# Kernel tuning notes

Hardware: AMD Instinct MI355X
Metric: run time of the kernel (lower is better)

## Reference

```python
import jax, jax.numpy as jnp
import numpy as np

N_NODES = 100000
N_EDGES = 20000
NNZ = 800000
D_IN = 256
D_OUT = 256


def _segment_mean(feats, seg_ids, num_segments):
    # feats: [nnz, d] gathered features; seg_ids: [nnz] target segment per entry
    s = jax.ops.segment_sum(feats, seg_ids, num_segments=num_segments)
    cnt = jax.ops.segment_sum(jnp.ones((seg_ids.shape[0],), feats.dtype), seg_ids,
                              num_segments=num_segments)
    return s / jnp.maximum(cnt, 1.0)[:, None]


def setup_inputs() -> dict:
    key = jax.random.key(0)
    k1, k2, k3, k4, k5 = jax.random.split(key, 5)
    X = jax.random.normal(k1, (N_NODES, D_IN), dtype=jnp.float32)
    W = jax.random.normal(k2, (D_IN, D_OUT), dtype=jnp.float32) * (1.0 / np.sqrt(D_IN))
    b = jax.random.normal(k3, (D_OUT,), dtype=jnp.float32) * 0.01
    vertex_idx = jax.random.randint(k4, (NNZ,), 0, N_NODES, dtype=jnp.int32)
    edge_idx = jax.random.randint(k5, (NNZ,), 0, N_EDGES, dtype=jnp.int32)
    return {"X": X, "W": W, "b": b, "vertex_idx": vertex_idx, "edge_idx": edge_idx}


def reference(X, W, b, vertex_idx, edge_idx):
    # theta: linear projection
    H = X @ W + b                                   # [N_NODES, D_OUT]
    # v2e mean: hyperedge feature = mean of incident vertex features
    Y = _segment_mean(H[vertex_idx], edge_idx, N_EDGES)   # [N_EDGES, D_OUT]
    # e2v mean: vertex feature = mean of incident hyperedge features
    X_ = _segment_mean(Y[edge_idx], vertex_idx, N_NODES)  # [N_NODES, D_OUT]
    # ReLU; dropout is identity in eval mode
    return jax.nn.relu(X_)
```

## Files before the change

kernel.cpp:

```cpp
#include <hip/hip_runtime.h>
#include <hip/hip_bf16.h>

constexpr int N_NODES = 100000;
constexpr int N_EDGES = 20000;
constexpr int NNZ     = 800000;
constexpr int D       = 256;

typedef unsigned short ushort_t;
typedef unsigned short ushort4v __attribute__((ext_vector_type(4)));
typedef unsigned short ushort8v __attribute__((ext_vector_type(8)));
typedef __bf16         bf16x8   __attribute__((ext_vector_type(8)));
typedef float          f32x4    __attribute__((ext_vector_type(4)));
typedef float          f32x8    __attribute__((ext_vector_type(8)));

static __device__ inline ushort_t f2bf(float f) {
  unsigned u = __builtin_bit_cast(unsigned, f);
  return (ushort_t)((u + 0x7FFFu + ((u >> 16) & 1u)) >> 16);
}

static __device__ inline f32x8 row_f32(const ushort_t* p) {
  bf16x8 b = __builtin_bit_cast(bf16x8, *(const ushort8v*)p);
  return __builtin_convertvector(b, f32x8);
}

static __device__ inline int bsum(unsigned long long x) {
  return (int)((x * 0x0101010101010101ULL) >> 56);
}

constexpr int HCHUNKS   = 8;
constexpr int CHUNK     = NNZ / HCHUNKS;
constexpr int CHUNK4    = CHUNK / 4;
constexpr int NH_RANGES = 5;
constexpr int NH_BINS   = N_NODES / NH_RANGES;
constexpr int NH_BLOCKS = NH_RANGES * HCHUNKS;
constexpr int EH_BLOCKS = HCHUNKS;
constexpr int HIST_BLOCKS  = NH_BLOCKS + EH_BLOCKS;
constexpr int TRANS_BLOCKS = 64;
constexpr int CAST_BLOCKS  = 6250;
constexpr int PREP_BLOCKS  = HIST_BLOCKS + TRANS_BLOCKS + CAST_BLOCKS;
constexpr int HWORDS = 5000;

__global__ __launch_bounds__(256) void prep_kernel(
    const float* __restrict__ X, const float* __restrict__ W,
    const int* __restrict__ vidx, const int* __restrict__ eidx,
    ushort_t* __restrict__ Xb, ushort_t* __restrict__ Wt,
    unsigned char* __restrict__ pe, unsigned char* __restrict__ pn,
    unsigned char* __restrict__ lre, unsigned char* __restrict__ lrn) {
  __shared__ unsigned int hist[HWORDS];
  const int blk = blockIdx.x, tid = threadIdx.x;
  if (blk < HIST_BLOCKS) {
    const bool is_n = blk < NH_BLOCKS;
    const int c  = is_n ? (blk & 7) : (blk - NH_BLOCKS);
    const int lo = is_n ? (blk >> 3) * NH_BINS : 0;
    const int* __restrict__ idx = is_n ? vidx : eidx;
    unsigned char* __restrict__ lr = is_n ? lrn : lre;
    for (int t = tid; t < HWORDS; t += 256) hist[t] = 0;
    __syncthreads();
    const int base4 = c * CHUNK4;
#pragma unroll 2
    for (int k = tid; k < CHUNK4; k += 256) {
      int i4 = base4 + k;
      int4 q = ((const int4*)idx)[i4];
      int vv[4] = {q.x, q.y, q.z, q.w};
#pragma unroll
      for (int j = 0; j < 4; ++j) {
        unsigned rel = (unsigned)(vv[j] - lo);
        if (rel < (unsigned)NH_BINS) {
          unsigned sh = 8u * (rel & 3u);
          unsigned old = atomicAdd(&hist[rel >> 2], 1u << sh);
          lr[(size_t)i4 * 4 + j] = (unsigned char)((old >> sh) & 0xFFu);
        }
      }
    }
    __syncthreads();
    unsigned char* __restrict__ pb = is_n ? pn : pe;
    for (int t = tid; t < NH_BINS; t += 256) {
      unsigned byte = (hist[t >> 2] >> (8u * (t & 3u))) & 0xFFu;
      pb[(size_t)(lo + t) * 8 + c] = (unsigned char)byte;
    }
  } else if (blk < HIST_BLOCKS + TRANS_BLOCKS) {
    int wb = blk - HIST_BLOCKS;
#pragma unroll
    for (int i = 0; i < 4; ++i) {
      int k = wb * 4 + i;
      Wt[(size_t)tid * 256 + k] = f2bf(W[(size_t)k * 256 + tid]);
    }
  } else {
    int cb = blk - HIST_BLOCKS - TRANS_BLOCKS;
#pragma unroll
    for (int q = 0; q < 4; ++q) {
      int idx4 = cb * 1024 + q * 256 + tid;
      float4 v = ((const float4*)X)[idx4];
      ushort4v o = { f2bf(v.x), f2bf(v.y), f2bf(v.z), f2bf(v.w) };
      *(ushort4v*)&Xb[(size_t)idx4 * 4] = o;
    }
  }
}

constexpr int SCAN_L    = N_EDGES + N_NODES;
constexpr int SCAN_TPB  = 1024;
constexpr int SCAN_EPT  = 4;
constexpr int SCAN_TILE = SCAN_TPB * SCAN_EPT;
constexpr int SCAN_NB   = (SCAN_L + SCAN_TILE - 1) / SCAN_TILE;

__global__ __launch_bounds__(1024) void scan_phaseA(
    const unsigned long long* __restrict__ pe,
    const unsigned long long* __restrict__ pn,
    int* __restrict__ comb, int* __restrict__ btot) {
  __shared__ int wsum[16];
  const int tid = threadIdx.x, lane = tid & 63, wid = tid >> 6;
  const int base = blockIdx.x * SCAN_TILE + tid * SCAN_EPT;
  int v[SCAN_EPT];
#pragma unroll
  for (int i = 0; i < SCAN_EPT; ++i) {
    int j = base + i;
    int x = 0;
    if (j < SCAN_L) x = bsum(j < N_EDGES ? pe[j] : pn[j - N_EDGES]);
    v[i] = x;
  }
  int tsum = v[0] + v[1] + v[2] + v[3];
  int x = tsum;
#pragma unroll
  for (int d = 1; d < 64; d <<= 1) {
    int y = __shfl_up(x, (unsigned)d, 64);
    if (lane >= d) x += y;
  }
  if (lane == 63) wsum[wid] = x;
  __syncthreads();
  if (wid == 0) {
    int s = (lane < 16) ? wsum[lane] : 0;
#pragma unroll
    for (int d = 1; d < 16; d <<= 1) {
      int y = __shfl_up(s, (unsigned)d, 64);
      if (lane >= d) s += y;
    }
    if (lane < 16) wsum[lane] = s;
  }
  __syncthreads();
  int texcl = ((wid == 0) ? 0 : wsum[wid - 1]) + (x - tsum);
  int run = texcl;
#pragma unroll
  for (int i = 0; i < SCAN_EPT; ++i) {
    int j = base + i;
    if (j < SCAN_L) comb[j] = run;
    run += v[i];
  }
  if (tid == 0) btot[blockIdx.x] = wsum[15];
}

__global__ __launch_bounds__(1024) void scan_phaseC(
    const int* __restrict__ comb, const int* __restrict__ btot,
    int* __restrict__ eoff, int* __restrict__ noff) {
  int add = 0;
  for (int bdx = 0; bdx < blockIdx.x; ++bdx) add += btot[bdx];
  const int base = blockIdx.x * SCAN_TILE + threadIdx.x * SCAN_EPT;
#pragma unroll
  for (int i = 0; i < SCAN_EPT; ++i) {
    int j = base + i;
    if (j < SCAN_L) {
      int val = comb[j] + add;
      if (j < N_EDGES) eoff[j] = val;
      else             noff[j - N_EDGES] = val - NNZ;
    }
  }
  if (blockIdx.x == 0 && threadIdx.x == 0) {
    eoff[N_EDGES] = NNZ;
    noff[N_NODES] = NNZ;
  }
}

__global__ __launch_bounds__(256) void scatter_calc(
    const int* __restrict__ vidx, const int* __restrict__ eidx,
    const int* __restrict__ eoff, const int* __restrict__ noff,
    const unsigned long long* __restrict__ pe,
    const unsigned long long* __restrict__ pn,
    const unsigned char* __restrict__ lre, const unsigned char* __restrict__ lrn,
    int* __restrict__ evals, int* __restrict__ nvals) {
  int i4 = blockIdx.x * 256 + threadIdx.x;
  if (i4 >= NNZ / 4) return;
  int c = i4 / CHUNK4;
  unsigned long long mask = (1ULL << (8 * c)) - 1ULL;
  int4 e4 = ((const int4*)eidx)[i4];
  int4 v4 = ((const int4*)vidx)[i4];
  unsigned le = *(const unsigned*)(lre + (size_t)i4 * 4);
  unsigned ln = *(const unsigned*)(lrn + (size_t)i4 * 4);
  int ee[4] = {e4.x, e4.y, e4.z, e4.w};
  int vv[4] = {v4.x, v4.y, v4.z, v4.w};
#pragma unroll
  for (int j = 0; j < 4; ++j) {
    int e = ee[j], v = vv[j];
    int re = (int)((le >> (8 * j)) & 0xFFu);
    int rn = (int)((ln >> (8 * j)) & 0xFFu);
    evals[eoff[e] + bsum(pe[e] & mask) + re] = v;
    nvals[noff[v] + bsum(pn[v] & mask) + rn] = e;
  }
}

__global__ __launch_bounds__(256) void v2e_mean(
    const ushort_t* __restrict__ Xb, const int* __restrict__ eoff,
    const int* __restrict__ evals, ushort_t* __restrict__ Xeb, int nseg) {
  int lane = threadIdx.x & 63;
  int half = lane >> 5, l32 = lane & 31;
  int seg  = blockIdx.x * 4 + (threadIdx.x >> 6);
  if (seg >= nseg) return;
  int s = eoff[seg], e = eoff[seg + 1];
  f32x8 acc = {0, 0, 0, 0, 0, 0, 0, 0};
  int j = s + half;
  for (; j + 6 < e; j += 8) {
    int r0 = evals[j], r1 = evals[j + 2], r2 = evals[j + 4], r3 = evals[j + 6];
    f32x8 f0 = row_f32(&Xb[(size_t)r0 * 256 + l32 * 8]);
    f32x8 f1 = row_f32(&Xb[(size_t)r1 * 256 + l32 * 8]);
    f32x8 f2 = row_f32(&Xb[(size_t)r2 * 256 + l32 * 8]);
    f32x8 f3 = row_f32(&Xb[(size_t)r3 * 256 + l32 * 8]);
    acc += (f0 + f1) + (f2 + f3);
  }
  for (; j < e; j += 2)
    acc += row_f32(&Xb[(size_t)evals[j] * 256 + l32 * 8]);
  float r[8];
#pragma unroll
  for (int i = 0; i < 8; ++i) r[i] = acc[i] + __shfl_down(acc[i], 32);
  if (half == 0) {
    float inv = 1.0f / (float)max(e - s, 1);
    ushort8v o;
#pragma unroll
    for (int i = 0; i < 8; ++i) o[i] = f2bf(r[i] * inv);
    *(ushort8v*)&Xeb[(size_t)seg * 256 + l32 * 8] = o;
  }
}

__global__ __launch_bounds__(256) void gemm_mfma(
    const ushort_t* __restrict__ A, const ushort_t* __restrict__ Wt,
    const float* __restrict__ bias, ushort_t* __restrict__ Ye) {
  const int w = threadIdx.x >> 6, lane = threadIdx.x & 63;
  const int m15 = lane & 15, q = lane >> 4;
  const int m0 = blockIdx.x * 16;
  const ushort_t* arow = A + (size_t)(m0 + m15) * 256 + q * 8;
  f32x4 acc[4] = { {0,0,0,0}, {0,0,0,0}, {0,0,0,0}, {0,0,0,0} };
  for (int k0 = 0; k0 < 256; k0 += 32) {
    bf16x8 af = __builtin_bit_cast(bf16x8, *(const ushort8v*)(arow + k0));
#pragma unroll
    for (int t = 0; t < 4; ++t) {
      const ushort_t* brow = Wt + (size_t)(w * 64 + t * 16 + m15) * 256 + k0 + q * 8;
      bf16x8 bf = __builtin_bit_cast(bf16x8, *(const ushort8v*)brow);
      acc[t] = __builtin_amdgcn_mfma_f32_16x16x32_bf16(af, bf, acc[t], 0, 0, 0);
    }
  }
#pragma unroll
  for (int t = 0; t < 4; ++t) {
    int col = w * 64 + t * 16 + m15;
    float bv = bias[col];
#pragma unroll
    for (int r = 0; r < 4; ++r) {
      int row = m0 + q * 4 + r;
      Ye[(size_t)row * 256 + col] = f2bf(acc[t][r] + bv);
    }
  }
}

__global__ __launch_bounds__(256) void e2v_mean_relu(
    const ushort_t* __restrict__ Yeb, const int* __restrict__ noff,
    const int* __restrict__ nvals, float* __restrict__ dst, int nseg) {
  int lane = threadIdx.x & 63;
  int half = lane >> 5, l32 = lane & 31;
  int seg  = blockIdx.x * 4 + (threadIdx.x >> 6);
  if (seg >= nseg) return;
  int s = noff[seg], e = noff[seg + 1];
  f32x8 acc = {0, 0, 0, 0, 0, 0, 0, 0};
  int j = s + half;
  for (; j + 6 < e; j += 8) {
    int r0 = nvals[j], r1 = nvals[j + 2], r2 = nvals[j + 4], r3 = nvals[j + 6];
    f32x8 f0 = row_f32(&Yeb[(size_t)r0 * 256 + l32 * 8]);
    f32x8 f1 = row_f32(&Yeb[(size_t)r1 * 256 + l32 * 8]);
    f32x8 f2 = row_f32(&Yeb[(size_t)r2 * 256 + l32 * 8]);
    f32x8 f3 = row_f32(&Yeb[(size_t)r3 * 256 + l32 * 8]);
    acc += (f0 + f1) + (f2 + f3);
  }
  for (; j < e; j += 2)
    acc += row_f32(&Yeb[(size_t)nvals[j] * 256 + l32 * 8]);
  float r[8];
#pragma unroll
  for (int i = 0; i < 8; ++i) r[i] = acc[i] + __shfl_down(acc[i], 32);
  if (half == 0) {
    float inv = 1.0f / (float)max(e - s, 1);
    float4 o0, o1;
    o0.x = fmaxf(r[0] * inv, 0.f); o0.y = fmaxf(r[1] * inv, 0.f);
    o0.z = fmaxf(r[2] * inv, 0.f); o0.w = fmaxf(r[3] * inv, 0.f);
    o1.x = fmaxf(r[4] * inv, 0.f); o1.y = fmaxf(r[5] * inv, 0.f);
    o1.z = fmaxf(r[6] * inv, 0.f); o1.w = fmaxf(r[7] * inv, 0.f);
    size_t base = (size_t)seg * 256 + l32 * 8;
    *(float4*)&dst[base]     = o0;
    *(float4*)&dst[base + 4] = o1;
  }
}

constexpr size_t OFF_XB    = 0;
constexpr size_t OFF_XEB   = OFF_XB  + (size_t)N_NODES * D * 2;
constexpr size_t OFF_YEB   = OFF_XEB + (size_t)N_EDGES * D * 2;
constexpr size_t OFF_WT    = OFF_YEB + (size_t)N_EDGES * D * 2;
constexpr size_t OFF_PE    = OFF_WT  + (size_t)D * D * 2;
constexpr size_t OFF_PN    = OFF_PE  + (size_t)N_EDGES * 8;
constexpr size_t OFF_LRE   = OFF_PN  + (size_t)N_NODES * 8;
constexpr size_t OFF_LRN   = OFF_LRE + (size_t)NNZ;
constexpr size_t OFF_EOFF  = OFF_LRN + (size_t)NNZ;
constexpr size_t OFF_NOFF  = OFF_EOFF + (size_t)(N_EDGES + 1 + 3) * 4;
constexpr size_t OFF_EVALS = OFF_NOFF + (size_t)(N_NODES + 1 + 3) * 4;
constexpr size_t OFF_NVALS = OFF_EVALS + (size_t)NNZ * 4;
constexpr size_t OFF_COMB  = OFF_NVALS + (size_t)NNZ * 4;
constexpr size_t OFF_BTOT  = OFF_COMB + (size_t)SCAN_L * 4;

extern "C" void kernel_launch(void* const* d_in, const int* in_sizes, int n_in,
                              void* d_out, int out_size, void* d_ws, size_t ws_size,
                              hipStream_t stream) {
  const float* X    = (const float*)d_in[0];
  const float* W    = (const float*)d_in[1];
  const float* b    = (const float*)d_in[2];
  const int*   vidx = (const int*)d_in[3];
  const int*   eidx = (const int*)d_in[4];
  float*       out  = (float*)d_out;

  char* ws = (char*)d_ws;
  ushort_t* Xb   = (ushort_t*)(ws + OFF_XB);
  ushort_t* Xeb  = (ushort_t*)(ws + OFF_XEB);
  ushort_t* Yeb  = (ushort_t*)(ws + OFF_YEB);
  ushort_t* Wt   = (ushort_t*)(ws + OFF_WT);
  unsigned char* pe_b = (unsigned char*)(ws + OFF_PE);
  unsigned char* pn_b = (unsigned char*)(ws + OFF_PN);
  unsigned long long* pe_u = (unsigned long long*)(ws + OFF_PE);
  unsigned long long* pn_u = (unsigned long long*)(ws + OFF_PN);
  unsigned char* lre = (unsigned char*)(ws + OFF_LRE);
  unsigned char* lrn = (unsigned char*)(ws + OFF_LRN);
  int* eoff  = (int*)(ws + OFF_EOFF);
  int* noff  = (int*)(ws + OFF_NOFF);
  int* evals = (int*)(ws + OFF_EVALS);
  int* nvals = (int*)(ws + OFF_NVALS);
  int* comb  = (int*)(ws + OFF_COMB);
  int* btot  = (int*)(ws + OFF_BTOT);


  prep_kernel<<<PREP_BLOCKS, 256, 0, stream>>>(X, W, vidx, eidx, Xb, Wt,
                                               pe_b, pn_b, lre, lrn);

  scan_phaseA<<<SCAN_NB, SCAN_TPB, 0, stream>>>(pe_u, pn_u, comb, btot);
  scan_phaseC<<<SCAN_NB, SCAN_TPB, 0, stream>>>(comb, btot, eoff, noff);

  scatter_calc<<<(NNZ / 4 + 255) / 256, 256, 0, stream>>>(
      vidx, eidx, eoff, noff, pe_u, pn_u, lre, lrn, evals, nvals);

  v2e_mean<<<(N_EDGES + 3) / 4, 256, 0, stream>>>(Xb, eoff, evals, Xeb, N_EDGES);

  gemm_mfma<<<N_EDGES / 16, 256, 0, stream>>>(Xeb, Wt, b, Yeb);

  e2v_mean_relu<<<(N_NODES + 3) / 4, 256, 0, stream>>>(Yeb, noff, nvals, out, N_NODES);
}
```

Measured before the change: 423.9 us.

## Widen histogram chunking to 32 and split segment-mean kernels into column quarters

Histogram construction now uses 32 chunks instead of 8, giving more blocks for the counting-sort prep. The per-(segment, chunk) prefix bytes grow to four u64 words, so the scan and scatter read and mask four words. Both segment-mean kernels are restructured: each wave handles a 64-column quarter of a segment, with 8 lanes per row and 8 rows in flight, and a 4x larger grid. This is meant to expose more parallelism and more memory-level parallelism on the gathers. The cost is more index re-reads, a larger prefix table, and extra shuffle reductions.

```diff
diff --git a/kernel.cpp b/kernel.cpp
--- a/kernel.cpp
+++ b/kernel.cpp
@@ -12,6 +12,8 @@
 typedef __bf16         bf16x8   __attribute__((ext_vector_type(8)));
 typedef float          f32x4    __attribute__((ext_vector_type(4)));
 typedef float          f32x8    __attribute__((ext_vector_type(8)));
+typedef unsigned long long u64;
+typedef unsigned long long u64x2 __attribute__((ext_vector_type(2)));
 
 static __device__ inline ushort_t f2bf(float f) {
   unsigned u = __builtin_bit_cast(unsigned, f);
@@ -23,13 +25,13 @@
   return __builtin_convertvector(b, f32x8);
 }
 
-static __device__ inline int bsum(unsigned long long x) {
+static __device__ inline int bsum(u64 x) {
   return (int)((x * 0x0101010101010101ULL) >> 56);
 }
 
-constexpr int HCHUNKS   = 8;
-constexpr int CHUNK     = NNZ / HCHUNKS;
-constexpr int CHUNK4    = CHUNK / 4;
+constexpr int HCHUNKS   = 32;
+constexpr int CHUNK4    = NNZ / 4 / HCHUNKS;
+constexpr int PWORDS    = HCHUNKS / 8;
 constexpr int NH_RANGES = 5;
 constexpr int NH_BINS   = N_NODES / NH_RANGES;
 constexpr int NH_BLOCKS = NH_RANGES * HCHUNKS;
@@ -50,14 +52,13 @@
   const int blk = blockIdx.x, tid = threadIdx.x;
   if (blk < HIST_BLOCKS) {
     const bool is_n = blk < NH_BLOCKS;
-    const int c  = is_n ? (blk & 7) : (blk - NH_BLOCKS);
-    const int lo = is_n ? (blk >> 3) * NH_BINS : 0;
+    const int c  = is_n ? (blk & (HCHUNKS - 1)) : (blk - NH_BLOCKS);
+    const int lo = is_n ? (blk >> 5) * NH_BINS : 0;
     const int* __restrict__ idx = is_n ? vidx : eidx;
     unsigned char* __restrict__ lr = is_n ? lrn : lre;
     for (int t = tid; t < HWORDS; t += 256) hist[t] = 0;
     __syncthreads();
     const int base4 = c * CHUNK4;
-#pragma unroll 2
     for (int k = tid; k < CHUNK4; k += 256) {
       int i4 = base4 + k;
       int4 q = ((const int4*)idx)[i4];
@@ -76,7 +77,7 @@
     unsigned char* __restrict__ pb = is_n ? pn : pe;
     for (int t = tid; t < NH_BINS; t += 256) {
       unsigned byte = (hist[t >> 2] >> (8u * (t & 3u))) & 0xFFu;
-      pb[(size_t)(lo + t) * 8 + c] = (unsigned char)byte;
+      pb[(size_t)(lo + t) * HCHUNKS + c] = (unsigned char)byte;
     }
   } else if (blk < HIST_BLOCKS + TRANS_BLOCKS) {
     int wb = blk - HIST_BLOCKS;
@@ -103,9 +104,14 @@
 constexpr int SCAN_TILE = SCAN_TPB * SCAN_EPT;
 constexpr int SCAN_NB   = (SCAN_L + SCAN_TILE - 1) / SCAN_TILE;
 
+static __device__ inline int bsum32(const u64* P) {
+  u64x2 a = *(const u64x2*)P;
+  u64x2 b = *(const u64x2*)(P + 2);
+  return bsum(a[0]) + bsum(a[1]) + bsum(b[0]) + bsum(b[1]);
+}
+
 __global__ __launch_bounds__(1024) void scan_phaseA(
-    const unsigned long long* __restrict__ pe,
-    const unsigned long long* __restrict__ pn,
+    const u64* __restrict__ pe, const u64* __restrict__ pn,
     int* __restrict__ comb, int* __restrict__ btot) {
   __shared__ int wsum[16];
   const int tid = threadIdx.x, lane = tid & 63, wid = tid >> 6;
@@ -115,7 +121,9 @@
   for (int i = 0; i < SCAN_EPT; ++i) {
     int j = base + i;
     int x = 0;
-    if (j < SCAN_L) x = bsum(j < N_EDGES ? pe[j] : pn[j - N_EDGES]);
+    if (j < SCAN_L)
+      x = bsum32(j < N_EDGES ? pe + (size_t)j * PWORDS
+                             : pn + (size_t)(j - N_EDGES) * PWORDS);
     v[i] = x;
   }
   int tsum = v[0] + v[1] + v[2] + v[3];
@@ -172,14 +180,18 @@
 __global__ __launch_bounds__(256) void scatter_calc(
     const int* __restrict__ vidx, const int* __restrict__ eidx,
     const int* __restrict__ eoff, const int* __restrict__ noff,
-    const unsigned long long* __restrict__ pe,
-    const unsigned long long* __restrict__ pn,
+    const u64* __restrict__ pe, const u64* __restrict__ pn,
     const unsigned char* __restrict__ lre, const unsigned char* __restrict__ lrn,
     int* __restrict__ evals, int* __restrict__ nvals) {
   int i4 = blockIdx.x * 256 + threadIdx.x;
   if (i4 >= NNZ / 4) return;
   int c = i4 / CHUNK4;
-  unsigned long long mask = (1ULL << (8 * c)) - 1ULL;
+  int w = c >> 3, sub = c & 7;
+  u64 mw = (1ULL << (8 * sub)) - 1ULL;
+  u64 m0 = (w > 0) ? ~0ULL : mw;
+  u64 m1 = (w > 1) ? ~0ULL : ((w == 1) ? mw : 0ULL);
+  u64 m2 = (w > 2) ? ~0ULL : ((w == 2) ? mw : 0ULL);
+  u64 m3 = (w == 3) ? mw : 0ULL;
   int4 e4 = ((const int4*)eidx)[i4];
   int4 v4 = ((const int4*)vidx)[i4];
   unsigned le = *(const unsigned*)(lre + (size_t)i4 * 4);
@@ -189,42 +201,46 @@
 #pragma unroll
   for (int j = 0; j < 4; ++j) {
     int e = ee[j], v = vv[j];
+    u64x2 ea = *(const u64x2*)(pe + (size_t)e * PWORDS);
+    u64x2 eb = *(const u64x2*)(pe + (size_t)e * PWORDS + 2);
+    u64x2 na = *(const u64x2*)(pn + (size_t)v * PWORDS);
+    u64x2 nb = *(const u64x2*)(pn + (size_t)v * PWORDS + 2);
+    int pre_e = bsum(ea[0] & m0) + bsum(ea[1] & m1) + bsum(eb[0] & m2) + bsum(eb[1] & m3);
+    int pre_n = bsum(na[0] & m0) + bsum(na[1] & m1) + bsum(nb[0] & m2) + bsum(nb[1] & m3);
     int re = (int)((le >> (8 * j)) & 0xFFu);
     int rn = (int)((ln >> (8 * j)) & 0xFFu);
-    evals[eoff[e] + bsum(pe[e] & mask) + re] = v;
-    nvals[noff[v] + bsum(pn[v] & mask) + rn] = e;
-  }
-}
-
-__global__ __launch_bounds__(256) void v2e_mean(
+    evals[eoff[e] + pre_e + re] = v;
+    nvals[noff[v] + pre_n + rn] = e;
+  }
+}
+
+constexpr int V2E_NBLK = N_EDGES / 4;
+__global__ __launch_bounds__(256) void v2e_mean_q(
     const ushort_t* __restrict__ Xb, const int* __restrict__ eoff,
-    const int* __restrict__ evals, ushort_t* __restrict__ Xeb, int nseg) {
-  int lane = threadIdx.x & 63;
-  int half = lane >> 5, l32 = lane & 31;
-  int seg  = blockIdx.x * 4 + (threadIdx.x >> 6);
-  if (seg >= nseg) return;
+    const int* __restrict__ evals, ushort_t* __restrict__ Xeb) {
+  int q    = blockIdx.x / V2E_NBLK;
+  int blk  = blockIdx.x - q * V2E_NBLK;
+  int wave = threadIdx.x >> 6, lane = threadIdx.x & 63;
+  int g = lane >> 3, l8 = lane & 7;
+  int seg = blk * 4 + wave;
   int s = eoff[seg], e = eoff[seg + 1];
+  const ushort_t* base = Xb + q * 64 + l8 * 8;
   f32x8 acc = {0, 0, 0, 0, 0, 0, 0, 0};
-  int j = s + half;
-  for (; j + 6 < e; j += 8) {
-    int r0 = evals[j], r1 = evals[j + 2], r2 = evals[j + 4], r3 = evals[j + 6];
-    f32x8 f0 = row_f32(&Xb[(size_t)r0 * 256 + l32 * 8]);
-    f32x8 f1 = row_f32(&Xb[(size_t)r1 * 256 + l32 * 8]);
-    f32x8 f2 = row_f32(&Xb[(size_t)r2 * 256 + l32 * 8]);
-    f32x8 f3 = row_f32(&Xb[(size_t)r3 * 256 + l32 * 8]);
-    acc += (f0 + f1) + (f2 + f3);
-  }
-  for (; j < e; j += 2)
-    acc += row_f32(&Xb[(size_t)evals[j] * 256 + l32 * 8]);
-  float r[8];
-#pragma unroll
-  for (int i = 0; i < 8; ++i) r[i] = acc[i] + __shfl_down(acc[i], 32);
-  if (half == 0) {
+#pragma unroll 2
+  for (int j = s + g; j < e; j += 8)
+    acc += row_f32(&base[(size_t)evals[j] * 256]);
+#pragma unroll
+  for (int i = 0; i < 8; ++i) {
+    acc[i] += __shfl_xor(acc[i], 8, 64);
+    acc[i] += __shfl_xor(acc[i], 16, 64);
+    acc[i] += __shfl_xor(acc[i], 32, 64);
+  }
+  if (g == 0) {
     float inv = 1.0f / (float)max(e - s, 1);
     ushort8v o;
 #pragma unroll
-    for (int i = 0; i < 8; ++i) o[i] = f2bf(r[i] * inv);
-    *(ushort8v*)&Xeb[(size_t)seg * 256 + l32 * 8] = o;
+    for (int i = 0; i < 8; ++i) o[i] = f2bf(acc[i] * inv);
+    *(ushort8v*)&Xeb[(size_t)seg * 256 + q * 64 + l8 * 8] = o;
   }
 }
 
@@ -257,39 +273,37 @@
   }
 }
 
-__global__ __launch_bounds__(256) void e2v_mean_relu(
+constexpr int E2V_NBLK = N_NODES / 4;
+__global__ __launch_bounds__(256) void e2v_mean_relu_q(
     const ushort_t* __restrict__ Yeb, const int* __restrict__ noff,
-    const int* __restrict__ nvals, float* __restrict__ dst, int nseg) {
-  int lane = threadIdx.x & 63;
-  int half = lane >> 5, l32 = lane & 31;
-  int seg  = blockIdx.x * 4 + (threadIdx.x >> 6);
-  if (seg >= nseg) return;
+    const int* __restrict__ nvals, float* __restrict__ dst) {
+  int q    = blockIdx.x / E2V_NBLK;
+  int blk  = blockIdx.x - q * E2V_NBLK;
+  int wave = threadIdx.x >> 6, lane = threadIdx.x & 63;
+  int g = lane >> 3, l8 = lane & 7;
+  int seg = blk * 4 + wave;
   int s = noff[seg], e = noff[seg + 1];
+  const ushort_t* base = Yeb + q * 64 + l8 * 8;
   f32x8 acc = {0, 0, 0, 0, 0, 0, 0, 0};
-  int j = s + half;
-  for (; j + 6 < e; j += 8) {
-    int r0 = nvals[j], r1 = nvals[j + 2], r2 = nvals[j + 4], r3 = nvals[j + 6];
-    f32x8 f0 = row_f32(&Yeb[(size_t)r0 * 256 + l32 * 8]);
-    f32x8 f1 = row_f32(&Yeb[(size_t)r1 * 256 + l32 * 8]);
-    f32x8 f2 = row_f32(&Yeb[(size_t)r2 * 256 + l32 * 8]);
-    f32x8 f3 = row_f32(&Yeb[(size_t)r3 * 256 + l32 * 8]);
-    acc += (f0 + f1) + (f2 + f3);
-  }
-  for (; j < e; j += 2)
-    acc += row_f32(&Yeb[(size_t)nvals[j] * 256 + l32 * 8]);
-  float r[8];
-#pragma unroll
-  for (int i = 0; i < 8; ++i) r[i] = acc[i] + __shfl_down(acc[i], 32);
-  if (half == 0) {
+#pragma unroll 2
+  for (int j = s + g; j < e; j += 8)
+    acc += row_f32(&base[(size_t)nvals[j] * 256]);
+#pragma unroll
+  for (int i = 0; i < 8; ++i) {
+    acc[i] += __shfl_xor(acc[i], 8, 64);
+    acc[i] += __shfl_xor(acc[i], 16, 64);
+    acc[i] += __shfl_xor(acc[i], 32, 64);
+  }
+  if (g == 0) {
     float inv = 1.0f / (float)max(e - s, 1);
     float4 o0, o1;
-    o0.x = fmaxf(r[0] * inv, 0.f); o0.y = fmaxf(r[1] * inv, 0.f);
-    o0.z = fmaxf(r[2] * inv, 0.f); o0.w = fmaxf(r[3] * inv, 0.f);
-    o1.x = fmaxf(r[4] * inv, 0.f); o1.y = fmaxf(r[5] * inv, 0.f);
-    o1.z = fmaxf(r[6] * inv, 0.f); o1.w = fmaxf(r[7] * inv, 0.f);
-    size_t base = (size_t)seg * 256 + l32 * 8;
-    *(float4*)&dst[base]     = o0;
-    *(float4*)&dst[base + 4] = o1;
+    o0.x = fmaxf(acc[0] * inv, 0.f); o0.y = fmaxf(acc[1] * inv, 0.f);
+    o0.z = fmaxf(acc[2] * inv, 0.f); o0.w = fmaxf(acc[3] * inv, 0.f);
+    o1.x = fmaxf(acc[4] * inv, 0.f); o1.y = fmaxf(acc[5] * inv, 0.f);
+    o1.z = fmaxf(acc[6] * inv, 0.f); o1.w = fmaxf(acc[7] * inv, 0.f);
+    size_t b = (size_t)seg * 256 + q * 64 + l8 * 8;
+    *(float4*)&dst[b]     = o0;
+    *(float4*)&dst[b + 4] = o1;
   }
 }
 
@@ -298,8 +312,8 @@
 constexpr size_t OFF_YEB   = OFF_XEB + (size_t)N_EDGES * D * 2;
 constexpr size_t OFF_WT    = OFF_YEB + (size_t)N_EDGES * D * 2;
 constexpr size_t OFF_PE    = OFF_WT  + (size_t)D * D * 2;
-constexpr size_t OFF_PN    = OFF_PE  + (size_t)N_EDGES * 8;
-constexpr size_t OFF_LRE   = OFF_PN  + (size_t)N_NODES * 8;
+constexpr size_t OFF_PN    = OFF_PE  + (size_t)N_EDGES * HCHUNKS;
+constexpr size_t OFF_LRE   = OFF_PN  + (size_t)N_NODES * HCHUNKS;
 constexpr size_t OFF_LRN   = OFF_LRE + (size_t)NNZ;
 constexpr size_t OFF_EOFF  = OFF_LRN + (size_t)NNZ;
 constexpr size_t OFF_NOFF  = OFF_EOFF + (size_t)(N_EDGES + 1 + 3) * 4;
@@ -325,8 +339,8 @@
   ushort_t* Wt   = (ushort_t*)(ws + OFF_WT);
   unsigned char* pe_b = (unsigned char*)(ws + OFF_PE);
   unsigned char* pn_b = (unsigned char*)(ws + OFF_PN);
-  unsigned long long* pe_u = (unsigned long long*)(ws + OFF_PE);
-  unsigned long long* pn_u = (unsigned long long*)(ws + OFF_PN);
+  u64* pe_u = (u64*)(ws + OFF_PE);
+  u64* pn_u = (u64*)(ws + OFF_PN);
   unsigned char* lre = (unsigned char*)(ws + OFF_LRE);
   unsigned char* lrn = (unsigned char*)(ws + OFF_LRN);
   int* eoff  = (int*)(ws + OFF_EOFF);
@@ -346,9 +360,9 @@
   scatter_calc<<<(NNZ / 4 + 255) / 256, 256, 0, stream>>>(
       vidx, eidx, eoff, noff, pe_u, pn_u, lre, lrn, evals, nvals);
 
-  v2e_mean<<<(N_EDGES + 3) / 4, 256, 0, stream>>>(Xb, eoff, evals, Xeb, N_EDGES);
+  v2e_mean_q<<<4 * V2E_NBLK, 256, 0, stream>>>(Xb, eoff, evals, Xeb);
 
   gemm_mfma<<<N_EDGES / 16, 256, 0, stream>>>(Xeb, Wt, b, Yeb);
 
-  e2v_mean_relu<<<(N_NODES + 3) / 4, 256, 0, stream>>>(Yeb, noff, nvals, out, N_NODES);
-}
+  e2v_mean_relu_q<<<4 * E2V_NBLK, 256, 0, stream>>>(Yeb, noff, nvals, out);
+}
```

Result: slower. 445.1 us (+5.0%).
